# Performance work log

Measured on AMD Instinct MI355X. Metric: run time of the kernel, lower is better.

The kernel has to match this reference:

```python
import jax, jax.numpy as jnp
import numpy as np

N, K = 262144, 8
IN_F, H_F, OUT_F = 16, 128, 16
NEG_SLOPE = 0.01  # torch LeakyReLU default


def setup_inputs() -> dict:
    key = jax.random.key(0)
    ks = jax.random.split(key, 10)
    h = jax.random.normal(ks[0], (N, IN_F), dtype=jnp.float32)
    pos = jax.random.uniform(ks[1], (N, 3), dtype=jnp.float32)
    nbr_idx = jax.random.randint(ks[2], (N, K), 0, N)

    def xavier(k, shape):
        fan_in, fan_out = shape[0], shape[1]
        a = jnp.sqrt(6.0 / (fan_in + fan_out))
        return jax.random.uniform(k, shape, jnp.float32, -a, a)

    W0 = xavier(ks[3], (K * IN_F, H_F))
    b0 = xavier(ks[4], (1, H_F))
    W1 = xavier(ks[5], (K * H_F, H_F))
    b1 = xavier(ks[6], (1, H_F))
    W2 = xavier(ks[7], (K * H_F, OUT_F))
    b2 = xavier(ks[8], (1, OUT_F))
    return {"h": h, "pos": pos, "nbr_idx": nbr_idx,
            "W0": W0, "b0": b0, "W1": W1, "b1": b1, "W2": W2, "b2": b2}


def _layer(h, pos, nbr_idx, W, b, activation):
    # gather neighbor messages and positions: [N, K, F], [N, K, 3]
    msgs = h[nbr_idx]
    src_pos = pos[nbr_idx]
    diff = pos[:, None, :] - src_pos                       # [N, K, 3]
    dist = jnp.sqrt(jnp.sum(diff * diff, axis=2, keepdims=True))  # [N, K, 1]
    dist = jnp.where(dist == 0, jnp.float32(0.5), dist)
    wow = (msgs / dist).reshape(h.shape[0], -1)            # [N, K*F]
    out = wow @ W + b
    if activation:
        out = jnp.where(out >= 0, out, NEG_SLOPE * out)
    return out


def reference(h, pos, nbr_idx, W0, b0, W1, b1, W2, b2):
    h1 = _layer(h, pos, nbr_idx, W0, b0, False)   # input layer
    h2 = _layer(h1, pos, nbr_idx, W1, b1, True)   # hidden layer (LeakyReLU)
    h3 = _layer(h2, pos, nbr_idx, W2, b2, False)  # output layer
    return h3
```

## Files before the change

### kernel.cpp

```cpp
#include <hip/hip_runtime.h>
#include <hip/hip_fp16.h>


typedef _Float16 f16x8 __attribute__((ext_vector_type(8)));
typedef float f32x4 __attribute__((ext_vector_type(4)));

#define NNODES 262144

__global__ __launch_bounds__(256) void conv_h_kernel(const float* __restrict__ h,
                                                     __half* __restrict__ h16, int n) {
    int i = blockIdx.x * 256 + threadIdx.x;
    if (i < n) h16[i] = __float2half(h[i]);
}

__global__ __launch_bounds__(256) void prep_edges_kernel(const float* __restrict__ pos,
                                                         const int* __restrict__ nbr,
                                                         __half* __restrict__ invd, int n_edges) {
    int e = blockIdx.x * 256 + threadIdx.x;
    if (e >= n_edges) return;
    int i = e >> 3;
    int n = nbr[e];
    float dx = pos[i * 3 + 0] - pos[n * 3 + 0];
    float dy = pos[i * 3 + 1] - pos[n * 3 + 1];
    float dz = pos[i * 3 + 2] - pos[n * 3 + 2];
    float d = sqrtf(dx * dx + dy * dy + dz * dz);
    if (d == 0.0f) d = 0.5f;
    invd[e] = __float2half((1.0f / d) * 0.00390625f);
}

__global__ __launch_bounds__(256) void shuffle_w_kernel(const float* __restrict__ W,
                                                        __half* __restrict__ Wf,
                                                        int KT, int FO) {
    int e = blockIdx.x * 256 + threadIdx.x;
    if (e >= KT * FO) return;
    int j = e & 7;
    int lane = (e >> 3) & 63;
    int rest = e >> 9;
    int NT = FO >> 4;
    int t = rest % NT;
    int s = rest / NT;
    int k = s * 32 + (lane >> 4) * 8 + j;
    int n = t * 16 + (lane & 15);
    Wf[e] = __float2half(W[k * FO + n]);
}

template <int F_IN, int F_OUT, int MT, bool LEAKY, bool OUT_F32>
__global__ __launch_bounds__(256, 2) void layer_kernel(
    const __half* __restrict__ hprev, const __half* __restrict__ invd,
    const int* __restrict__ nbr, const __half* __restrict__ Wf,
    const float* __restrict__ bias, void* __restrict__ outp) {
    constexpr int NT = F_OUT / 16;
    constexpr bool CHUNKED = (F_IN == 128 && F_OUT == 128);
    constexpr int BS_HALVES = CHUNKED ? 32768 : 16384;

    __shared__ __align__(16) __half Bs[BS_HALVES];

    const int tid = threadIdx.x;
    const int wave = tid >> 6;
    const int lane = tid & 63;
    const int quad = lane >> 4;
    const int lmod = lane & 15;
    const int mbase = blockIdx.x * (64 * MT) + wave * 16 + lmod;

    int idx[MT][8];
    f16x8 invr[MT];
#pragma unroll
    for (int mt = 0; mt < MT; ++mt) {
        const int m = mbase + mt * 64;
        const int4* nrow = (const int4*)(nbr + (size_t)m * 8);
        const int4 iA = nrow[0];
        const int4 iB = nrow[1];
        idx[mt][0] = iA.x; idx[mt][1] = iA.y; idx[mt][2] = iA.z; idx[mt][3] = iA.w;
        idx[mt][4] = iB.x; idx[mt][5] = iB.y; idx[mt][6] = iB.z; idx[mt][7] = iB.w;
        invr[mt] = *(const f16x8*)(invd + (size_t)m * 8);
    }

    f32x4 acc[MT][NT];
#pragma unroll
    for (int mt = 0; mt < MT; ++mt)
#pragma unroll
        for (int t = 0; t < NT; ++t) acc[mt][t] = f32x4{0.f, 0.f, 0.f, 0.f};

    if constexpr (F_IN == 128) {
        f16x8 a[8][4];
#pragma unroll
        for (int nb = 0; nb < 8; ++nb) {
            const size_t base = (size_t)idx[0][nb] * 128;
#pragma unroll
            for (int ks = 0; ks < 4; ++ks)
                a[nb][ks] = *(const f16x8*)(hprev + base + ks * 32 + quad * 8);
        }

        if constexpr (CHUNKED) {
            {
                const uint4* src = (const uint4*)Wf;
                uint4* dst = (uint4*)Bs;
#pragma unroll
                for (int i = 0; i < 8; ++i) dst[i * 256 + tid] = src[i * 256 + tid];
            }
            __syncthreads();

#pragma unroll
            for (int nb = 0; nb < 8; ++nb) {
                uint4 btmp[8];
                if (nb < 7) {
                    const uint4* src = (const uint4*)(Wf + (size_t)(nb + 1) * 16384);
#pragma unroll
                    for (int i = 0; i < 8; ++i) btmp[i] = src[i * 256 + tid];
                }

                const __half* bb = Bs + (nb & 1) * 16384;
#pragma unroll
                for (int ks = 0; ks < 4; ++ks) {
                    const f16x8 as = a[nb][ks] * invr[0][nb];
#pragma unroll
                    for (int t = 0; t < NT; ++t) {
                        f16x8 b = *(const f16x8*)(bb + ((size_t)(ks * NT + t) * 64 + lane) * 8);
                        acc[0][t] = __builtin_amdgcn_mfma_f32_16x16x32_f16(as, b, acc[0][t], 0, 0, 0);
                    }
                }

                if (nb < 7) {
                    uint4* dst = (uint4*)(Bs + ((nb + 1) & 1) * 16384);
#pragma unroll
                    for (int i = 0; i < 8; ++i) dst[i * 256 + tid] = btmp[i];
                    __syncthreads();
                }
            }
        } else {
            {
                const uint4* src = (const uint4*)Wf;
                uint4* dst = (uint4*)Bs;
#pragma unroll
                for (int i = 0; i < 8; ++i) dst[i * 256 + tid] = src[i * 256 + tid];
            }
            __syncthreads();

#pragma unroll
            for (int nb = 0; nb < 8; ++nb) {
#pragma unroll
                for (int ks = 0; ks < 4; ++ks) {
                    const f16x8 as = a[nb][ks] * invr[0][nb];
                    const int s = nb * 4 + ks;
#pragma unroll
                    for (int t = 0; t < NT; ++t) {
                        f16x8 b = *(const f16x8*)(Bs + ((size_t)(s * NT + t) * 64 + lane) * 8);
                        acc[0][t] = __builtin_amdgcn_mfma_f32_16x16x32_f16(as, b, acc[0][t], 0, 0, 0);
                    }
                }
            }
        }
    } else {
        {
            const uint4* src = (const uint4*)Wf;
            uint4* dst = (uint4*)Bs;
#pragma unroll
            for (int i = 0; i < 8; ++i) dst[i * 256 + tid] = src[i * 256 + tid];
        }
        __syncthreads();

#pragma unroll
        for (int s = 0; s < 4; ++s) {
            const int nb = 2 * s + (quad >> 1);
            f16x8 as[MT];
#pragma unroll
            for (int mt = 0; mt < MT; ++mt) {
                f16x8 av = *(const f16x8*)(hprev + (size_t)idx[mt][nb] * 16 + (quad & 1) * 8);
                as[mt] = av * invr[mt][nb];
            }
#pragma unroll
            for (int t = 0; t < NT; ++t) {
                f16x8 b = *(const f16x8*)(Bs + ((size_t)(s * NT + t) * 64 + lane) * 8);
#pragma unroll
                for (int mt = 0; mt < MT; ++mt)
                    acc[mt][t] = __builtin_amdgcn_mfma_f32_16x16x32_f16(as[mt], b, acc[mt][t], 0, 0, 0);
            }
        }
    }

#pragma unroll
    for (int mt = 0; mt < MT; ++mt) {
        const int rbase = blockIdx.x * (64 * MT) + mt * 64 + wave * 16 + quad * 4;
#pragma unroll
        for (int t = 0; t < NT; ++t) {
            const int col = t * 16 + lmod;
            const float bv = bias[col];
#pragma unroll
            for (int rr = 0; rr < 4; ++rr) {
                const int grow = rbase + rr;
                float v = acc[mt][t][rr] * 256.0f + bv;
                if (LEAKY) v = (v >= 0.f) ? v : 0.01f * v;
                if (OUT_F32)
                    ((float*)outp)[(size_t)grow * F_OUT + col] = v;
                else
                    ((__half*)outp)[(size_t)grow * F_OUT + col] = __float2half(v);
            }
        }
    }
}

extern "C" void kernel_launch(void* const* d_in, const int* in_sizes, int n_in,
                              void* d_out, int out_size, void* d_ws, size_t ws_size,
                              hipStream_t stream) {
    const float* h   = (const float*)d_in[0];
    const float* pos = (const float*)d_in[1];
    const int*   nbr = (const int*)d_in[2];
    const float* W0  = (const float*)d_in[3];
    const float* b0  = (const float*)d_in[4];
    const float* W1  = (const float*)d_in[5];
    const float* b1  = (const float*)d_in[6];
    const float* W2  = (const float*)d_in[7];
    const float* b2  = (const float*)d_in[8];

    const int N = NNODES;

    char* w = (char*)d_ws;
    __half* h1 = (__half*)w;
    __half* h2 = (__half*)(w + (size_t)67108864);
    __half* invd2 = (__half*)w;
    __half* W2f2  = (__half*)(w + (size_t)4194304);

    char* ob = (char*)d_out;
    __half* invd = (__half*)(ob + 0);
    __half* h16  = (__half*)(ob + 4194304);
    __half* W0f  = (__half*)(ob + 12582912);
    __half* W1f  = (__half*)(ob + 12615680);
    __half* W2f  = (__half*)(ob + 12877824);

    conv_h_kernel<<<(N * 16 + 255) / 256, 256, 0, stream>>>(h, h16, N * 16);
    prep_edges_kernel<<<(N * 8 + 255) / 256, 256, 0, stream>>>(pos, nbr, invd, N * 8);
    shuffle_w_kernel<<<(128 * 128 + 255) / 256, 256, 0, stream>>>(W0, W0f, 128, 128);
    shuffle_w_kernel<<<(1024 * 128 + 255) / 256, 256, 0, stream>>>(W1, W1f, 1024, 128);
    shuffle_w_kernel<<<(1024 * 16 + 255) / 256, 256, 0, stream>>>(W2, W2f, 1024, 16);

    layer_kernel<16, 128, 2, false, false><<<N / 128, 256, 0, stream>>>(h16, invd, nbr, W0f, b0, h1);
    layer_kernel<128, 128, 1, true, false><<<N / 64, 256, 0, stream>>>(h1, invd, nbr, W1f, b1, h2);

    hipMemcpyAsync(invd2, invd, 4194304, hipMemcpyDeviceToDevice, stream);
    hipMemcpyAsync(W2f2, W2f, 32768, hipMemcpyDeviceToDevice, stream);

    layer_kernel<128, 16, 1, false, true><<<N / 64, 256, 0, stream>>>(h2, invd2, nbr, W2f2, b2, d_out);
}
```

Before: 373.7 us.

## Split layer kernel into specialized per-layer kernels with pipelined gathers

Replaces the templated layer kernel with three dedicated kernels. The hidden layer now stages gathered, distance-scaled neighbor rows in double-buffered shared memory and holds each wave's column slice of the weights in registers, prefetching the next neighbor and its weights while MFMAs run. The output layer keeps a three-slot rotating register buffer of gathered rows instead of loading all eight neighbors up front, which should lower register pressure and overlap loads with compute. The hidden-layer kernel is now 64 rows per block with 3-block occupancy, at the cost of more synchronization per neighbor step.

```diff
diff --git a/kernel.cpp b/kernel.cpp
--- a/kernel.cpp
+++ b/kernel.cpp
@@ -44,28 +44,23 @@
     Wf[e] = __float2half(W[k * FO + n]);
 }
 
-template <int F_IN, int F_OUT, int MT, bool LEAKY, bool OUT_F32>
-__global__ __launch_bounds__(256, 2) void layer_kernel(
+__global__ __launch_bounds__(256) void layer0_kernel(
     const __half* __restrict__ hprev, const __half* __restrict__ invd,
     const int* __restrict__ nbr, const __half* __restrict__ Wf,
-    const float* __restrict__ bias, void* __restrict__ outp) {
-    constexpr int NT = F_OUT / 16;
-    constexpr bool CHUNKED = (F_IN == 128 && F_OUT == 128);
-    constexpr int BS_HALVES = CHUNKED ? 32768 : 16384;
-
-    __shared__ __align__(16) __half Bs[BS_HALVES];
+    const float* __restrict__ bias, __half* __restrict__ outp) {
+    __shared__ __align__(16) __half Bs[16384];
 
     const int tid = threadIdx.x;
     const int wave = tid >> 6;
     const int lane = tid & 63;
     const int quad = lane >> 4;
     const int lmod = lane & 15;
-    const int mbase = blockIdx.x * (64 * MT) + wave * 16 + lmod;
-
-    int idx[MT][8];
-    f16x8 invr[MT];
-#pragma unroll
-    for (int mt = 0; mt < MT; ++mt) {
+    const int mbase = blockIdx.x * 128 + wave * 16 + lmod;
+
+    int idx[2][8];
+    f16x8 invr[2];
+#pragma unroll
+    for (int mt = 0; mt < 2; ++mt) {
         const int m = mbase + mt * 64;
         const int4* nrow = (const int4*)(nbr + (size_t)m * 8);
         const int4 iA = nrow[0];
@@ -75,128 +70,220 @@
         invr[mt] = *(const f16x8*)(invd + (size_t)m * 8);
     }
 
-    f32x4 acc[MT][NT];
-#pragma unroll
-    for (int mt = 0; mt < MT; ++mt)
-#pragma unroll
-        for (int t = 0; t < NT; ++t) acc[mt][t] = f32x4{0.f, 0.f, 0.f, 0.f};
-
-    if constexpr (F_IN == 128) {
-        f16x8 a[8][4];
-#pragma unroll
-        for (int nb = 0; nb < 8; ++nb) {
-            const size_t base = (size_t)idx[0][nb] * 128;
-#pragma unroll
-            for (int ks = 0; ks < 4; ++ks)
-                a[nb][ks] = *(const f16x8*)(hprev + base + ks * 32 + quad * 8);
-        }
-
-        if constexpr (CHUNKED) {
-            {
-                const uint4* src = (const uint4*)Wf;
-                uint4* dst = (uint4*)Bs;
-#pragma unroll
-                for (int i = 0; i < 8; ++i) dst[i * 256 + tid] = src[i * 256 + tid];
-            }
-            __syncthreads();
-
-#pragma unroll
-            for (int nb = 0; nb < 8; ++nb) {
-                uint4 btmp[8];
-                if (nb < 7) {
-                    const uint4* src = (const uint4*)(Wf + (size_t)(nb + 1) * 16384);
-#pragma unroll
-                    for (int i = 0; i < 8; ++i) btmp[i] = src[i * 256 + tid];
-                }
-
-                const __half* bb = Bs + (nb & 1) * 16384;
-#pragma unroll
-                for (int ks = 0; ks < 4; ++ks) {
-                    const f16x8 as = a[nb][ks] * invr[0][nb];
-#pragma unroll
-                    for (int t = 0; t < NT; ++t) {
-                        f16x8 b = *(const f16x8*)(bb + ((size_t)(ks * NT + t) * 64 + lane) * 8);
-                        acc[0][t] = __builtin_amdgcn_mfma_f32_16x16x32_f16(as, b, acc[0][t], 0, 0, 0);
-                    }
-                }
-
-                if (nb < 7) {
-                    uint4* dst = (uint4*)(Bs + ((nb + 1) & 1) * 16384);
-#pragma unroll
-                    for (int i = 0; i < 8; ++i) dst[i * 256 + tid] = btmp[i];
-                    __syncthreads();
-                }
-            }
-        } else {
-            {
-                const uint4* src = (const uint4*)Wf;
-                uint4* dst = (uint4*)Bs;
-#pragma unroll
-                for (int i = 0; i < 8; ++i) dst[i * 256 + tid] = src[i * 256 + tid];
-            }
-            __syncthreads();
-
-#pragma unroll
-            for (int nb = 0; nb < 8; ++nb) {
-#pragma unroll
-                for (int ks = 0; ks < 4; ++ks) {
-                    const f16x8 as = a[nb][ks] * invr[0][nb];
-                    const int s = nb * 4 + ks;
-#pragma unroll
-                    for (int t = 0; t < NT; ++t) {
-                        f16x8 b = *(const f16x8*)(Bs + ((size_t)(s * NT + t) * 64 + lane) * 8);
-                        acc[0][t] = __builtin_amdgcn_mfma_f32_16x16x32_f16(as, b, acc[0][t], 0, 0, 0);
-                    }
-                }
-            }
-        }
-    } else {
-        {
-            const uint4* src = (const uint4*)Wf;
-            uint4* dst = (uint4*)Bs;
-#pragma unroll
-            for (int i = 0; i < 8; ++i) dst[i * 256 + tid] = src[i * 256 + tid];
-        }
-        __syncthreads();
-
-#pragma unroll
-        for (int s = 0; s < 4; ++s) {
-            const int nb = 2 * s + (quad >> 1);
-            f16x8 as[MT];
-#pragma unroll
-            for (int mt = 0; mt < MT; ++mt) {
-                f16x8 av = *(const f16x8*)(hprev + (size_t)idx[mt][nb] * 16 + (quad & 1) * 8);
-                as[mt] = av * invr[mt][nb];
-            }
-#pragma unroll
-            for (int t = 0; t < NT; ++t) {
-                f16x8 b = *(const f16x8*)(Bs + ((size_t)(s * NT + t) * 64 + lane) * 8);
-#pragma unroll
-                for (int mt = 0; mt < MT; ++mt)
-                    acc[mt][t] = __builtin_amdgcn_mfma_f32_16x16x32_f16(as[mt], b, acc[mt][t], 0, 0, 0);
-            }
-        }
-    }
-
-#pragma unroll
-    for (int mt = 0; mt < MT; ++mt) {
-        const int rbase = blockIdx.x * (64 * MT) + mt * 64 + wave * 16 + quad * 4;
-#pragma unroll
-        for (int t = 0; t < NT; ++t) {
+    f32x4 acc[2][8];
+#pragma unroll
+    for (int mt = 0; mt < 2; ++mt)
+#pragma unroll
+        for (int t = 0; t < 8; ++t) acc[mt][t] = f32x4{0.f, 0.f, 0.f, 0.f};
+
+    {
+        const uint4* src = (const uint4*)Wf;
+        uint4* dst = (uint4*)Bs;
+#pragma unroll
+        for (int i = 0; i < 8; ++i) dst[i * 256 + tid] = src[i * 256 + tid];
+    }
+    __syncthreads();
+
+#pragma unroll
+    for (int s = 0; s < 4; ++s) {
+        const int nb = 2 * s + (quad >> 1);
+        f16x8 as[2];
+#pragma unroll
+        for (int mt = 0; mt < 2; ++mt) {
+            f16x8 av = *(const f16x8*)(hprev + (size_t)idx[mt][nb] * 16 + (quad & 1) * 8);
+            as[mt] = av * invr[mt][nb];
+        }
+#pragma unroll
+        for (int t = 0; t < 8; ++t) {
+            f16x8 b = *(const f16x8*)(Bs + ((size_t)(s * 8 + t) * 64 + lane) * 8);
+#pragma unroll
+            for (int mt = 0; mt < 2; ++mt)
+                acc[mt][t] = __builtin_amdgcn_mfma_f32_16x16x32_f16(as[mt], b, acc[mt][t], 0, 0, 0);
+        }
+    }
+
+#pragma unroll
+    for (int mt = 0; mt < 2; ++mt) {
+        const int rbase = blockIdx.x * 128 + mt * 64 + wave * 16 + quad * 4;
+#pragma unroll
+        for (int t = 0; t < 8; ++t) {
             const int col = t * 16 + lmod;
             const float bv = bias[col];
 #pragma unroll
             for (int rr = 0; rr < 4; ++rr) {
-                const int grow = rbase + rr;
                 float v = acc[mt][t][rr] * 256.0f + bv;
-                if (LEAKY) v = (v >= 0.f) ? v : 0.01f * v;
-                if (OUT_F32)
-                    ((float*)outp)[(size_t)grow * F_OUT + col] = v;
-                else
-                    ((__half*)outp)[(size_t)grow * F_OUT + col] = __float2half(v);
+                outp[(size_t)(rbase + rr) * 128 + col] = __float2half(v);
             }
         }
     }
+}
+
+__global__ __launch_bounds__(256, 3) void layer1_kernel(
+    const __half* __restrict__ hprev, const __half* __restrict__ invd,
+    const int* __restrict__ nbr, const __half* __restrict__ Wf,
+    const float* __restrict__ bias, __half* __restrict__ outp) {
+    __shared__ __align__(16) __half As[2][64][136];
+
+    const int tid = threadIdx.x;
+    const int wave = tid >> 6;
+    const int lane = tid & 63;
+    const int quad = lane >> 4;
+    const int lmod = lane & 15;
+    const int rowblk = blockIdx.x * 64;
+    const int seg = lmod;
+
+    int srow[4], grow_[4];
+#pragma unroll
+    for (int i = 0; i < 4; ++i) { srow[i] = wave * 16 + i * 4 + quad; grow_[i] = rowblk + srow[i]; }
+
+    f16x8 invS[4];
+#pragma unroll
+    for (int i = 0; i < 4; ++i) invS[i] = *(const f16x8*)(invd + (size_t)grow_[i] * 8);
+
+    int idx0[4], idxP[2][4];
+#pragma unroll
+    for (int i = 0; i < 4; ++i) idx0[i] = nbr[(size_t)grow_[i] * 8 + 0];
+#pragma unroll
+    for (int i = 0; i < 4; ++i) idxP[1][i] = nbr[(size_t)grow_[i] * 8 + 1];
+
+    const __half* WfB = Wf + ((size_t)(wave * 2) * 64 + lane) * 8;
+
+    f16x8 Bc[4][2], Bn[4][2];
+#pragma unroll
+    for (int ks = 0; ks < 4; ++ks)
+#pragma unroll
+        for (int tl = 0; tl < 2; ++tl)
+            Bc[ks][tl] = *(const f16x8*)(WfB + (size_t)(ks * 8 + tl) * 512);
+
+    f16x8 ga[4];
+#pragma unroll
+    for (int i = 0; i < 4; ++i)
+        ga[i] = *(const f16x8*)(hprev + (size_t)idx0[i] * 128 + seg * 8);
+#pragma unroll
+    for (int i = 0; i < 4; ++i) {
+        f16x8 v = ga[i] * invS[i][0];
+        *(f16x8*)(&As[0][srow[i]][seg * 8]) = v;
+    }
+    __syncthreads();
+
+    f32x4 acc[4][2];
+#pragma unroll
+    for (int m = 0; m < 4; ++m) { acc[m][0] = f32x4{0.f,0.f,0.f,0.f}; acc[m][1] = f32x4{0.f,0.f,0.f,0.f}; }
+
+#pragma unroll
+    for (int nb = 0; nb < 8; ++nb) {
+        const int cur = nb & 1;
+        if (nb < 7) {
+#pragma unroll
+            for (int i = 0; i < 4; ++i)
+                ga[i] = *(const f16x8*)(hprev + (size_t)idxP[(nb + 1) & 1][i] * 128 + seg * 8);
+        }
+        if (nb < 6) {
+#pragma unroll
+            for (int i = 0; i < 4; ++i)
+                idxP[nb & 1][i] = nbr[(size_t)grow_[i] * 8 + nb + 2];
+        }
+        if (nb < 7) {
+#pragma unroll
+            for (int ks = 0; ks < 4; ++ks)
+#pragma unroll
+                for (int tl = 0; tl < 2; ++tl)
+                    Bn[ks][tl] = *(const f16x8*)(WfB + (size_t)(((nb + 1) * 4 + ks) * 8 + tl) * 512);
+        }
+#pragma unroll
+        for (int m = 0; m < 4; ++m) {
+#pragma unroll
+            for (int ks = 0; ks < 4; ++ks) {
+                f16x8 a = *(const f16x8*)(&As[cur][m * 16 + lmod][ks * 32 + quad * 8]);
+                acc[m][0] = __builtin_amdgcn_mfma_f32_16x16x32_f16(a, Bc[ks][0], acc[m][0], 0, 0, 0);
+                acc[m][1] = __builtin_amdgcn_mfma_f32_16x16x32_f16(a, Bc[ks][1], acc[m][1], 0, 0, 0);
+            }
+        }
+        if (nb < 7) {
+#pragma unroll
+            for (int i = 0; i < 4; ++i) {
+                f16x8 v = ga[i] * invS[i][nb + 1];
+                *(f16x8*)(&As[cur ^ 1][srow[i]][seg * 8]) = v;
+            }
+#pragma unroll
+            for (int ks = 0; ks < 4; ++ks) { Bc[ks][0] = Bn[ks][0]; Bc[ks][1] = Bn[ks][1]; }
+            __syncthreads();
+        }
+    }
+
+#pragma unroll
+    for (int m = 0; m < 4; ++m) {
+#pragma unroll
+        for (int tl = 0; tl < 2; ++tl) {
+            const int col = wave * 32 + tl * 16 + lmod;
+            const float bv = bias[col];
+#pragma unroll
+            for (int rr = 0; rr < 4; ++rr) {
+                const int grow = rowblk + m * 16 + quad * 4 + rr;
+                float v = acc[m][tl][rr] * 256.0f + bv;
+                v = (v >= 0.f) ? v : 0.01f * v;
+                outp[(size_t)grow * 128 + col] = __float2half(v);
+            }
+        }
+    }
+}
+
+__global__ __launch_bounds__(256) void layer2_kernel(
+    const __half* __restrict__ hprev, const __half* __restrict__ invd,
+    const int* __restrict__ nbr, const __half* __restrict__ Wf,
+    const float* __restrict__ bias, float* __restrict__ outp) {
+    __shared__ __align__(16) __half Bs[16384];
+
+    const int tid = threadIdx.x;
+    const int wave = tid >> 6;
+    const int lane = tid & 63;
+    const int quad = lane >> 4;
+    const int lmod = lane & 15;
+    const int m = blockIdx.x * 64 + wave * 16 + lmod;
+
+    const int4* nrow = (const int4*)(nbr + (size_t)m * 8);
+    const int4 iA = nrow[0];
+    const int4 iB = nrow[1];
+    const int idx[8] = {iA.x, iA.y, iA.z, iA.w, iB.x, iB.y, iB.z, iB.w};
+    const f16x8 invr = *(const f16x8*)(invd + (size_t)m * 8);
+
+    {
+        const uint4* src = (const uint4*)Wf;
+        uint4* dst = (uint4*)Bs;
+#pragma unroll
+        for (int i = 0; i < 8; ++i) dst[i * 256 + tid] = src[i * 256 + tid];
+    }
+    __syncthreads();
+
+    f16x8 a[3][4];
+#pragma unroll
+    for (int d = 0; d < 3; ++d)
+#pragma unroll
+        for (int ks = 0; ks < 4; ++ks)
+            a[d][ks] = *(const f16x8*)(hprev + (size_t)idx[d] * 128 + ks * 32 + quad * 8);
+
+    f32x4 acc = f32x4{0.f, 0.f, 0.f, 0.f};
+#pragma unroll
+    for (int nb = 0; nb < 8; ++nb) {
+        const int slot = nb % 3;
+#pragma unroll
+        for (int ks = 0; ks < 4; ++ks) {
+            f16x8 as = a[slot][ks] * invr[nb];
+            f16x8 b = *(const f16x8*)(Bs + ((size_t)(nb * 4 + ks) * 64 + lane) * 8);
+            acc = __builtin_amdgcn_mfma_f32_16x16x32_f16(as, b, acc, 0, 0, 0);
+        }
+        if (nb < 5) {
+#pragma unroll
+            for (int ks = 0; ks < 4; ++ks)
+                a[slot][ks] = *(const f16x8*)(hprev + (size_t)idx[nb + 3] * 128 + ks * 32 + quad * 8);
+        }
+    }
+
+    const int rbase = blockIdx.x * 64 + wave * 16 + quad * 4;
+    const float bv = bias[lmod];
+#pragma unroll
+    for (int rr = 0; rr < 4; ++rr)
+        outp[(size_t)(rbase + rr) * 16 + lmod] = acc[rr] * 256.0f + bv;
 }
 
 extern "C" void kernel_launch(void* const* d_in, const int* in_sizes, int n_in,
@@ -233,11 +320,11 @@
     shuffle_w_kernel<<<(1024 * 128 + 255) / 256, 256, 0, stream>>>(W1, W1f, 1024, 128);
     shuffle_w_kernel<<<(1024 * 16 + 255) / 256, 256, 0, stream>>>(W2, W2f, 1024, 16);
 
-    layer_kernel<16, 128, 2, false, false><<<N / 128, 256, 0, stream>>>(h16, invd, nbr, W0f, b0, h1);
-    layer_kernel<128, 128, 1, true, false><<<N / 64, 256, 0, stream>>>(h1, invd, nbr, W1f, b1, h2);
-
-    hipMemcpyAsync(invd2, invd, 4194304, hipMemcpyDeviceToDevice, stream);
-    hipMemcpyAsync(W2f2, W2f, 32768, hipMemcpyDeviceToDevice, stream);
-
-    layer_kernel<128, 16, 1, false, true><<<N / 64, 256, 0, stream>>>(h2, invd2, nbr, W2f2, b2, d_out);
-}
+    layer0_kernel<<<N / 128, 256, 0, stream>>>(h16, invd, nbr, W0f, b0, h1);
+    layer1_kernel<<<N / 64, 256, 0, stream>>>(h1, invd, nbr, W1f, b1, h2);
+
+    (void)hipMemcpyAsync(invd2, invd, 4194304, hipMemcpyDeviceToDevice, stream);
+    (void)hipMemcpyAsync(W2f2, W2f, 32768, hipMemcpyDeviceToDevice, stream);
+
+    layer2_kernel<<<N / 64, 256, 0, stream>>>(h2, invd2, nbr, W2f2, b2, (float*)d_out);
+}
```

After: 333.3 us. -10.8%, faster.
